# Performance work log

Hardware: AMD Instinct MI355X
Metric: run time of the kernel (lower is better)

## Reference

```python
import jax, jax.numpy as jnp
import numpy as np

LN_EPS = 1e-12


def setup_inputs() -> dict:
    key = jax.random.key(0)
    ks = jax.random.split(key, 5)
    E, H, I = 8, 768, 3072
    T = 2048  # tokens per expert (capacity-balanced)
    N = E * T
    return {
        "hidden_states": jax.random.normal(ks[0], (N, H), jnp.float32),
        "w1": jax.random.normal(ks[1], (E, H, I), jnp.float32) * (H ** -0.5),
        "b1": jax.random.normal(ks[2], (E, I), jnp.float32) * 0.02,
        "w2": jax.random.normal(ks[3], (E, I, H), jnp.float32) * (I ** -0.5),
        "b2": jax.random.normal(ks[4], (E, H), jnp.float32) * 0.02,
        "ln_gamma": jnp.ones((H,), jnp.float32),
        "ln_beta": jnp.zeros((H,), jnp.float32),
        "tokens_per_expert": T,
    }


def reference(hidden_states, w1, b1, w2, b2, ln_gamma, ln_beta, tokens_per_expert):
    E = w1.shape[0]
    N, H = hidden_states.shape
    # tokens are pre-sorted by expert; equal capacity per expert -> grouped GEMM
    x = hidden_states.reshape(E, tokens_per_expert, H)  # [E, T, H]
    # dense1 + exact GELU (BERT ACT2FN['gelu'])
    inter = jax.nn.gelu(jnp.einsum("eth,ehi->eti", x, w1) + b1[:, None, :],
                        approximate=False)  # [E, T, I]
    # dense2
    out = jnp.einsum("eti,eih->eth", inter, w2) + b2[:, None, :]  # [E, T, H]
    # dropout is identity in eval mode; residual + LayerNorm
    y = out.reshape(N, H) + hidden_states
    mean = jnp.mean(y, axis=-1, keepdims=True)
    var = jnp.mean(jnp.square(y - mean), axis=-1, keepdims=True)
    return (y - mean) * jax.lax.rsqrt(var + LN_EPS) * ln_gamma + ln_beta
```

## Files before the change

kernel.cpp:

```cpp
#include <hip/hip_runtime.h>
#include <hip/hip_bf16.h>
#include <math.h>

#define E_   8
#define H_   768
#define I_   3072
#define T_   2048
#define NTOK (E_ * T_)

typedef __attribute__((ext_vector_type(8))) short bf16x8;
typedef __attribute__((ext_vector_type(4))) float f32x4;

typedef __attribute__((address_space(3))) void lds_void;
typedef const __attribute__((address_space(1))) void gl_void;

__device__ __forceinline__ void gload16(const void* g, void* l) {
  __builtin_amdgcn_global_load_lds((gl_void*)g, (lds_void*)l, 16, 0, 0);
}

#define FENCE() asm volatile("" ::: "memory")
#define BAR()                         \
  do {                                \
    FENCE();                          \
    __builtin_amdgcn_s_barrier();     \
    FENCE();                          \
  } while (0)
#define VMWAIT(n) asm volatile("s_waitcnt vmcnt(" #n ")" ::: "memory")

#define MFMA16(a, b, c) __builtin_amdgcn_mfma_f32_16x16x32_bf16(a, b, c, 0, 0, 0)

__device__ __forceinline__ float gelu_fast(float v) {
  float inner = v * fmaf(v * v, 0.044715f, 1.0f);
  float e = __builtin_amdgcn_exp2f(inner * -2.3022082f);
  return v * __builtin_amdgcn_rcpf(1.0f + e);
}

__global__ __launch_bounds__(256) void cvt_bf16_kernel(
    const float* __restrict__ in, __hip_bfloat16* __restrict__ out) {
  int i = (blockIdx.x * 256 + threadIdx.x) * 4;
  float4 v = *(const float4*)(in + i);
  __align__(8) __hip_bfloat16 t[4];
  t[0] = __float2bfloat16(v.x);
  t[1] = __float2bfloat16(v.y);
  t[2] = __float2bfloat16(v.z);
  t[3] = __float2bfloat16(v.w);
  *(ushort4*)(out + i) = *(const ushort4*)t;
}

__global__ __launch_bounds__(256) void transpose_cvt_kernel(
    const float* __restrict__ src, __hip_bfloat16* __restrict__ dst,
    int R, int C) {
  __shared__ __hip_bfloat16 tile[64][65];
  int e  = blockIdx.z;
  int c0 = blockIdx.x * 64;
  int r0 = blockIdx.y * 64;
  const float* s = src + (size_t)e * R * C;
  __hip_bfloat16* d = dst + (size_t)e * R * C;
  int tx = threadIdx.x & 63, ty = threadIdx.x >> 6;
#pragma unroll
  for (int r = ty; r < 64; r += 4)
    tile[r][tx] = __float2bfloat16(s[(size_t)(r0 + r) * C + c0 + tx]);
  __syncthreads();
#pragma unroll
  for (int r = ty; r < 64; r += 4)
    d[(size_t)(c0 + r) * R + r0 + tx] = tile[tx][r];
}

template <int K, int N, bool GELU>
__global__ __launch_bounds__(512, 2) void gemm8p_kernel(
    const __hip_bfloat16* __restrict__ A,
    const __hip_bfloat16* __restrict__ B,
    const float* __restrict__ bias,
    __hip_bfloat16* __restrict__ out) {
  constexpr int MT = T_ / 256;
  constexpr int NT = N / 256;
  constexpr int KT = K / 64;

  __shared__ __hip_bfloat16 sA[2][2][128][64];
  __shared__ __hip_bfloat16 sB[2][2][128][64];

  int nwg = gridDim.x;
  int b0  = blockIdx.x;
  int bid = (b0 & 7) * (nwg >> 3) + (b0 >> 3);

  int e   = bid / (MT * NT);
  int rr_ = bid % (MT * NT);
  int bm  = rr_ / NT;
  int bn  = rr_ % NT;

  const __hip_bfloat16* Ae = A + (size_t)e * T_ * K + (size_t)bm * 256 * K;
  const __hip_bfloat16* Be = B + (size_t)e * N  * K + (size_t)bn * 256 * K;

  int tid  = threadIdx.x;
  int lane = tid & 63;
  int wid  = tid >> 6;
  int wr   = wid >> 2;
  int wc   = wid & 3;
  int l15  = lane & 15;
  int l16h = lane >> 4;

  int i0 = tid, i1 = 512 + tid;
  int lr0 = i0 >> 3, c80 = i0 & 7, cg0 = c80 ^ (lr0 & 7);
  int lr1 = i1 >> 3, c81 = i1 & 7, cg1 = c81 ^ (lr1 & 7);
  int rA0 = ((lr0 >> 6) << 7) | (lr0 & 63);
  int rA1 = ((lr1 >> 6) << 7) | (lr1 & 63);
  int rB0 = ((lr0 >> 5) << 6) | (lr0 & 31);
  int rB1 = ((lr1 >> 5) << 6) | (lr1 & 31);

  auto stageA = [&](int buf, int h, int kt) {
    const __hip_bfloat16* g = Ae + (size_t)kt * 64;
    gload16(g + (size_t)(rA0 | (h << 6)) * K + cg0 * 8, &sA[buf][h][lr0][c80 * 8]);
    gload16(g + (size_t)(rA1 | (h << 6)) * K + cg1 * 8, &sA[buf][h][lr1][c81 * 8]);
  };
  auto stageB = [&](int buf, int h, int kt) {
    const __hip_bfloat16* g = Be + (size_t)kt * 64;
    gload16(g + (size_t)(rB0 | (h << 5)) * K + cg0 * 8, &sB[buf][h][lr0][c80 * 8]);
    gload16(g + (size_t)(rB1 | (h << 5)) * K + cg1 * 8, &sB[buf][h][lr1][c81 * 8]);
  };

  int laBase = wr * 64 + l15;
  int lbBase = wc * 32 + l15;
  int s7   = l15 & 7;
  int cgr0 = ((0 | l16h) ^ s7) * 8;
  int cgr1 = ((4 | l16h) ^ s7) * 8;

  f32x4 acc[8][4] = {};
  bf16x8 af[4][2], bfv[4][2];

  stageA(0, 0, 0);
  stageB(0, 0, 0);
  stageB(0, 1, 0);
  stageA(0, 1, 0);

  auto ktile = [&](int kt, int p, bool pf) {
    VMWAIT(4);
    BAR();
#pragma unroll
    for (int mf = 0; mf < 4; ++mf) {
      int la = laBase + mf * 16;
      af[mf][0] = *(const bf16x8*)&sA[p][0][la][cgr0];
      af[mf][1] = *(const bf16x8*)&sA[p][0][la][cgr1];
    }
#pragma unroll
    for (int nf = 0; nf < 2; ++nf) {
      int lb = lbBase + nf * 16;
      bfv[nf][0] = *(const bf16x8*)&sB[p][0][lb][cgr0];
      bfv[nf][1] = *(const bf16x8*)&sB[p][0][lb][cgr1];
    }
    if (pf) stageA(p ^ 1, 0, kt + 1);
    __builtin_amdgcn_s_setprio(1);
#pragma unroll
    for (int mf = 0; mf < 4; ++mf)
#pragma unroll
      for (int nf = 0; nf < 2; ++nf) {
        acc[mf][nf] = MFMA16(af[mf][0], bfv[nf][0], acc[mf][nf]);
        acc[mf][nf] = MFMA16(af[mf][1], bfv[nf][1], acc[mf][nf]);
      }
    __builtin_amdgcn_s_setprio(0);
    if (pf) { VMWAIT(4); } else { VMWAIT(2); }
    BAR();
#pragma unroll
    for (int nf = 0; nf < 2; ++nf) {
      int lb = lbBase + nf * 16;
      bfv[2 + nf][0] = *(const bf16x8*)&sB[p][1][lb][cgr0];
      bfv[2 + nf][1] = *(const bf16x8*)&sB[p][1][lb][cgr1];
    }
    if (pf) stageB(p ^ 1, 0, kt + 1);
    __builtin_amdgcn_s_setprio(1);
#pragma unroll
    for (int mf = 0; mf < 4; ++mf)
#pragma unroll
      for (int nf = 2; nf < 4; ++nf) {
        acc[mf][nf] = MFMA16(af[mf][0], bfv[nf][0], acc[mf][nf]);
        acc[mf][nf] = MFMA16(af[mf][1], bfv[nf][1], acc[mf][nf]);
      }
    __builtin_amdgcn_s_setprio(0);
    if (pf) { VMWAIT(4); } else { VMWAIT(0); }
    BAR();
#pragma unroll
    for (int mf = 0; mf < 4; ++mf) {
      int la = laBase + mf * 16;
      af[mf][0] = *(const bf16x8*)&sA[p][1][la][cgr0];
      af[mf][1] = *(const bf16x8*)&sA[p][1][la][cgr1];
    }
    if (pf) stageB(p ^ 1, 1, kt + 1);
    __builtin_amdgcn_s_setprio(1);
#pragma unroll
    for (int mf = 0; mf < 4; ++mf)
#pragma unroll
      for (int nf = 2; nf < 4; ++nf) {
        acc[4 + mf][nf] = MFMA16(af[mf][0], bfv[nf][0], acc[4 + mf][nf]);
        acc[4 + mf][nf] = MFMA16(af[mf][1], bfv[nf][1], acc[4 + mf][nf]);
      }
    __builtin_amdgcn_s_setprio(0);
    if (pf) stageA(p ^ 1, 1, kt + 1);
    __builtin_amdgcn_s_setprio(1);
#pragma unroll
    for (int mf = 0; mf < 4; ++mf)
#pragma unroll
      for (int nf = 0; nf < 2; ++nf) {
        acc[4 + mf][nf] = MFMA16(af[mf][0], bfv[nf][0], acc[4 + mf][nf]);
        acc[4 + mf][nf] = MFMA16(af[mf][1], bfv[nf][1], acc[4 + mf][nf]);
      }
    __builtin_amdgcn_s_setprio(0);
  };

  int p = 0;
  for (int kt = 0; kt < KT - 1; ++kt) {
    ktile(kt, p, true);
    p ^= 1;
  }
  ktile(KT - 1, p, false);

  const float* be = bias + (size_t)e * N + bn * 256;
  __hip_bfloat16* oe =
      out + (size_t)e * T_ * N + (size_t)(bm * 256) * N + bn * 256;
  int r4 = l16h * 4;
#pragma unroll
  for (int mi = 0; mi < 8; ++mi) {
    int mh = mi >> 2, mf = mi & 3;
    int rowb = wr * 128 + mh * 64 + mf * 16 + r4;
#pragma unroll
    for (int nf = 0; nf < 4; ++nf) {
      int cc   = wc * 64 + nf * 16 + l15;
      float bv = be[cc];
#pragma unroll
      for (int r = 0; r < 4; ++r) {
        float v = acc[mi][nf][r] + bv;
        if (GELU) v = gelu_fast(v);
        oe[(size_t)(rowb + r) * N + cc] = __float2bfloat16(v);
      }
    }
  }
}

__global__ __launch_bounds__(256) void ln_kernel(
    const __hip_bfloat16* __restrict__ yraw, const float* __restrict__ x,
    const float* __restrict__ gamma, const float* __restrict__ beta,
    float* __restrict__ out) {
  int row  = blockIdx.x;
  int tid  = threadIdx.x;
  int lane = tid & 63, wid = tid >> 6;
  const __hip_bfloat16* yr = yraw + (size_t)row * H_;
  const float* xr = x + (size_t)row * H_;

  float v[3];
  float s = 0.f, s2 = 0.f;
#pragma unroll
  for (int j = 0; j < 3; ++j) {
    int c   = tid + j * 256;
    float t = __bfloat162float(yr[c]) + xr[c];
    v[j] = t;
    s += t;
    s2 += t * t;
  }
#pragma unroll
  for (int o = 32; o > 0; o >>= 1) {
    s  += __shfl_down(s, o);
    s2 += __shfl_down(s2, o);
  }
  __shared__ float ls[4], ls2[4];
  if (lane == 0) { ls[wid] = s; ls2[wid] = s2; }
  __syncthreads();
  float tot  = ls[0] + ls[1] + ls[2] + ls[3];
  float tot2 = ls2[0] + ls2[1] + ls2[2] + ls2[3];
  float mean = tot * (1.0f / 768.0f);
  float var  = tot2 * (1.0f / 768.0f) - mean * mean;
  float inv  = rsqrtf(var + 1e-12f);
  float* orow = out + (size_t)row * H_;
#pragma unroll
  for (int j = 0; j < 3; ++j) {
    int c = tid + j * 256;
    orow[c] = (v[j] - mean) * inv * gamma[c] + beta[c];
  }
}

extern "C" void kernel_launch(void* const* d_in, const int* in_sizes, int n_in,
                              void* d_out, int out_size, void* d_ws,
                              size_t ws_size, hipStream_t stream) {
  const float* x     = (const float*)d_in[0];
  const float* w1    = (const float*)d_in[1];
  const float* b1    = (const float*)d_in[2];
  const float* w2    = (const float*)d_in[3];
  const float* b2    = (const float*)d_in[4];
  const float* gamma = (const float*)d_in[5];
  const float* beta  = (const float*)d_in[6];
  float* out = (float*)d_out;

  char* ws = (char*)d_ws;
  __hip_bfloat16* w1t   = (__hip_bfloat16*)(ws);
  __hip_bfloat16* w2t   = (__hip_bfloat16*)(ws + 37748736);
  __hip_bfloat16* x_bf  = (__hip_bfloat16*)(ws + 75497472);
  __hip_bfloat16* inter = (__hip_bfloat16*)(ws + 100663296);
  __hip_bfloat16* yraw  = x_bf;

  cvt_bf16_kernel<<<(NTOK * H_) / (256 * 4), 256, 0, stream>>>(x, x_bf);
  transpose_cvt_kernel<<<dim3(I_ / 64, H_ / 64, E_), 256, 0, stream>>>(
      w1, w1t, H_, I_);
  transpose_cvt_kernel<<<dim3(H_ / 64, I_ / 64, E_), 256, 0, stream>>>(
      w2, w2t, I_, H_);
  gemm8p_kernel<H_, I_, true>
      <<<E_ * (T_ / 256) * (I_ / 256), 512, 0, stream>>>(x_bf, w1t, b1, inter);
  gemm8p_kernel<I_, H_, false>
      <<<E_ * (T_ / 256) * (H_ / 256), 512, 0, stream>>>(inter, w2t, b2, yraw);
  ln_kernel<<<NTOK, 256, 0, stream>>>(yraw, x, gamma, beta, out);
}
```

Measured before the change: 253.0 us.

## Restructure GEMM k-tile into two phases and use 256x192 tiles for dense2

The GEMM k-tile loop is reorganised from four phases with three barriers into two phases with two barriers. The whole B tile is staged at once and each wave's B fragments stay in registers across both A halves. The N tile width becomes a template parameter, and the second GEMM uses 192-wide tiles so its grid grows from 192 to 256 workgroups, better filling the CUs. The costs are more live B-fragment registers, different wait counts for prefetch overlap, and a smaller N tile for dense2, which lowers reuse.

Result: no change. 252.8 us (-0.1%).

```diff
diff --git a/kernel.cpp b/kernel.cpp
--- a/kernel.cpp
+++ b/kernel.cpp
@@ -66,18 +66,21 @@
     d[(size_t)(c0 + r) * R + r0 + tx] = tile[tx][r];
 }
 
-template <int K, int N, bool GELU>
-__global__ __launch_bounds__(512, 2) void gemm8p_kernel(
+template <int K, int N, int BN, bool GELU>
+__global__ __launch_bounds__(512, 2) void gemm2p_kernel(
     const __hip_bfloat16* __restrict__ A,
     const __hip_bfloat16* __restrict__ B,
     const float* __restrict__ bias,
     __hip_bfloat16* __restrict__ out) {
   constexpr int MT = T_ / 256;
-  constexpr int NT = N / 256;
+  constexpr int NT = N / BN;
   constexpr int KT = K / 64;
+  constexpr int NF = BN / 64;
+  constexpr int WCW = BN / 4;
+  constexpr int BPASS = BN / 64;
 
   __shared__ __hip_bfloat16 sA[2][2][128][64];
-  __shared__ __hip_bfloat16 sB[2][2][128][64];
+  __shared__ __hip_bfloat16 sB[2][BN][64];
 
   int nwg = gridDim.x;
   int b0  = blockIdx.x;
@@ -89,7 +92,7 @@
   int bn  = rr_ % NT;
 
   const __hip_bfloat16* Ae = A + (size_t)e * T_ * K + (size_t)bm * 256 * K;
-  const __hip_bfloat16* Be = B + (size_t)e * N  * K + (size_t)bn * 256 * K;
+  const __hip_bfloat16* Be = B + (size_t)e * N  * K + (size_t)bn * BN * K;
 
   int tid  = threadIdx.x;
   int lane = tid & 63;
@@ -104,36 +107,38 @@
   int lr1 = i1 >> 3, c81 = i1 & 7, cg1 = c81 ^ (lr1 & 7);
   int rA0 = ((lr0 >> 6) << 7) | (lr0 & 63);
   int rA1 = ((lr1 >> 6) << 7) | (lr1 & 63);
-  int rB0 = ((lr0 >> 5) << 6) | (lr0 & 31);
-  int rB1 = ((lr1 >> 5) << 6) | (lr1 & 31);
 
   auto stageA = [&](int buf, int h, int kt) {
     const __hip_bfloat16* g = Ae + (size_t)kt * 64;
     gload16(g + (size_t)(rA0 | (h << 6)) * K + cg0 * 8, &sA[buf][h][lr0][c80 * 8]);
     gload16(g + (size_t)(rA1 | (h << 6)) * K + cg1 * 8, &sA[buf][h][lr1][c81 * 8]);
   };
-  auto stageB = [&](int buf, int h, int kt) {
+  auto stageB = [&](int buf, int kt) {
     const __hip_bfloat16* g = Be + (size_t)kt * 64;
-    gload16(g + (size_t)(rB0 | (h << 5)) * K + cg0 * 8, &sB[buf][h][lr0][c80 * 8]);
-    gload16(g + (size_t)(rB1 | (h << 5)) * K + cg1 * 8, &sB[buf][h][lr1][c81 * 8]);
+#pragma unroll
+    for (int q = 0; q < BPASS; ++q) {
+      int idx = q * 512 + tid;
+      int lr = idx >> 3, c8 = idx & 7;
+      int cg = c8 ^ (lr & 7);
+      gload16(g + (size_t)lr * K + cg * 8, &sB[buf][lr][c8 * 8]);
+    }
   };
 
   int laBase = wr * 64 + l15;
-  int lbBase = wc * 32 + l15;
+  int lbBase = wc * WCW + l15;
   int s7   = l15 & 7;
   int cgr0 = ((0 | l16h) ^ s7) * 8;
   int cgr1 = ((4 | l16h) ^ s7) * 8;
 
-  f32x4 acc[8][4] = {};
-  bf16x8 af[4][2], bfv[4][2];
+  f32x4 acc[8][NF] = {};
+  bf16x8 af[4][2], bfv[NF][2];
 
   stageA(0, 0, 0);
-  stageB(0, 0, 0);
-  stageB(0, 1, 0);
+  stageB(0, 0);
   stageA(0, 1, 0);
 
   auto ktile = [&](int kt, int p, bool pf) {
-    VMWAIT(4);
+    VMWAIT(2);
     BAR();
 #pragma unroll
     for (int mf = 0; mf < 4; ++mf) {
@@ -142,40 +147,29 @@
       af[mf][1] = *(const bf16x8*)&sA[p][0][la][cgr1];
     }
 #pragma unroll
-    for (int nf = 0; nf < 2; ++nf) {
+    for (int nf = 0; nf < NF; ++nf) {
       int lb = lbBase + nf * 16;
-      bfv[nf][0] = *(const bf16x8*)&sB[p][0][lb][cgr0];
-      bfv[nf][1] = *(const bf16x8*)&sB[p][0][lb][cgr1];
-    }
-    if (pf) stageA(p ^ 1, 0, kt + 1);
+      bfv[nf][0] = *(const bf16x8*)&sB[p][lb][cgr0];
+      bfv[nf][1] = *(const bf16x8*)&sB[p][lb][cgr1];
+    }
+    if (pf) {
+      stageA(p ^ 1, 0, kt + 1);
+      stageB(p ^ 1, kt + 1);
+    }
     __builtin_amdgcn_s_setprio(1);
 #pragma unroll
     for (int mf = 0; mf < 4; ++mf)
 #pragma unroll
-      for (int nf = 0; nf < 2; ++nf) {
+      for (int nf = 0; nf < NF; ++nf) {
         acc[mf][nf] = MFMA16(af[mf][0], bfv[nf][0], acc[mf][nf]);
         acc[mf][nf] = MFMA16(af[mf][1], bfv[nf][1], acc[mf][nf]);
       }
     __builtin_amdgcn_s_setprio(0);
-    if (pf) { VMWAIT(4); } else { VMWAIT(2); }
-    BAR();
-#pragma unroll
-    for (int nf = 0; nf < 2; ++nf) {
-      int lb = lbBase + nf * 16;
-      bfv[2 + nf][0] = *(const bf16x8*)&sB[p][1][lb][cgr0];
-      bfv[2 + nf][1] = *(const bf16x8*)&sB[p][1][lb][cgr1];
-    }
-    if (pf) stageB(p ^ 1, 0, kt + 1);
-    __builtin_amdgcn_s_setprio(1);
-#pragma unroll
-    for (int mf = 0; mf < 4; ++mf)
-#pragma unroll
-      for (int nf = 2; nf < 4; ++nf) {
-        acc[mf][nf] = MFMA16(af[mf][0], bfv[nf][0], acc[mf][nf]);
-        acc[mf][nf] = MFMA16(af[mf][1], bfv[nf][1], acc[mf][nf]);
-      }
-    __builtin_amdgcn_s_setprio(0);
-    if (pf) { VMWAIT(4); } else { VMWAIT(0); }
+    if (pf) {
+      if constexpr (BN == 256) { VMWAIT(6); } else { VMWAIT(5); }
+    } else {
+      VMWAIT(0);
+    }
     BAR();
 #pragma unroll
     for (int mf = 0; mf < 4; ++mf) {
@@ -183,22 +177,12 @@
       af[mf][0] = *(const bf16x8*)&sA[p][1][la][cgr0];
       af[mf][1] = *(const bf16x8*)&sA[p][1][la][cgr1];
     }
-    if (pf) stageB(p ^ 1, 1, kt + 1);
-    __builtin_amdgcn_s_setprio(1);
-#pragma unroll
-    for (int mf = 0; mf < 4; ++mf)
-#pragma unroll
-      for (int nf = 2; nf < 4; ++nf) {
-        acc[4 + mf][nf] = MFMA16(af[mf][0], bfv[nf][0], acc[4 + mf][nf]);
-        acc[4 + mf][nf] = MFMA16(af[mf][1], bfv[nf][1], acc[4 + mf][nf]);
-      }
-    __builtin_amdgcn_s_setprio(0);
     if (pf) stageA(p ^ 1, 1, kt + 1);
     __builtin_amdgcn_s_setprio(1);
 #pragma unroll
     for (int mf = 0; mf < 4; ++mf)
 #pragma unroll
-      for (int nf = 0; nf < 2; ++nf) {
+      for (int nf = 0; nf < NF; ++nf) {
         acc[4 + mf][nf] = MFMA16(af[mf][0], bfv[nf][0], acc[4 + mf][nf]);
         acc[4 + mf][nf] = MFMA16(af[mf][1], bfv[nf][1], acc[4 + mf][nf]);
       }
@@ -212,17 +196,17 @@
   }
   ktile(KT - 1, p, false);
 
-  const float* be = bias + (size_t)e * N + bn * 256;
+  const float* be = bias + (size_t)e * N + bn * BN;
   __hip_bfloat16* oe =
-      out + (size_t)e * T_ * N + (size_t)(bm * 256) * N + bn * 256;
+      out + (size_t)e * T_ * N + (size_t)(bm * 256) * N + bn * BN;
   int r4 = l16h * 4;
 #pragma unroll
   for (int mi = 0; mi < 8; ++mi) {
     int mh = mi >> 2, mf = mi & 3;
     int rowb = wr * 128 + mh * 64 + mf * 16 + r4;
 #pragma unroll
-    for (int nf = 0; nf < 4; ++nf) {
-      int cc   = wc * 64 + nf * 16 + l15;
+    for (int nf = 0; nf < NF; ++nf) {
+      int cc   = wc * WCW + nf * 16 + l15;
       float bv = be[cc];
 #pragma unroll
       for (int r = 0; r < 4; ++r) {
@@ -299,9 +283,9 @@
       w1, w1t, H_, I_);
   transpose_cvt_kernel<<<dim3(H_ / 64, I_ / 64, E_), 256, 0, stream>>>(
       w2, w2t, I_, H_);
-  gemm8p_kernel<H_, I_, true>
+  gemm2p_kernel<H_, I_, 256, true>
       <<<E_ * (T_ / 256) * (I_ / 256), 512, 0, stream>>>(x_bf, w1t, b1, inter);
-  gemm8p_kernel<I_, H_, false>
-      <<<E_ * (T_ / 256) * (H_ / 256), 512, 0, stream>>>(inter, w2t, b2, yraw);
+  gemm2p_kernel<I_, H_, 192, false>
+      <<<E_ * (T_ / 256) * (H_ / 192), 512, 0, stream>>>(inter, w2t, b2, yraw);
   ln_kernel<<<NTOK, 256, 0, stream>>>(yraw, x, gamma, beta, out);
 }
```

## Restructure GEMM main loop into two-tile unrolled ping-pong schedule with explicit waits

Applied to the files above, without the earlier changes.

Replaces the single-k-tile loop with a two-k-tile unrolled iteration. Prefetch is issued for both buffers, and each quadrant of MFMAs is bracketed by barriers and explicit lgkmcnt waits with sched_barrier, in the style of an 8-wave ping-pong schedule. The goal is tighter overlap of global-to-LDS loads, LDS reads and MFMA, and more even instruction interleaving across the waves of the workgroup. Separately, the transpose kernel's write phase now stores two bf16 values per thread as ushort2, giving wider coalesced stores. The extra barriers could add sync overhead, and the kernel now requires an even k-tile count.

Result: slower. 258.3 us (+2.1%).

```diff
diff --git a/kernel.cpp b/kernel.cpp
--- a/kernel.cpp
+++ b/kernel.cpp
@@ -26,6 +26,11 @@
     FENCE();                          \
   } while (0)
 #define VMWAIT(n) asm volatile("s_waitcnt vmcnt(" #n ")" ::: "memory")
+#define LGKM0()                                  \
+  do {                                           \
+    asm volatile("s_waitcnt lgkmcnt(0)" ::: "memory"); \
+    __builtin_amdgcn_sched_barrier(0);           \
+  } while (0)
 
 #define MFMA16(a, b, c) __builtin_amdgcn_mfma_f32_16x16x32_bf16(a, b, c, 0, 0, 0)
 
@@ -61,20 +66,28 @@
   for (int r = ty; r < 64; r += 4)
     tile[r][tx] = __float2bfloat16(s[(size_t)(r0 + r) * C + c0 + tx]);
   __syncthreads();
-#pragma unroll
-  for (int r = ty; r < 64; r += 4)
-    d[(size_t)(c0 + r) * R + r0 + tx] = tile[tx][r];
+  int tx2 = threadIdx.x & 31;
+  int ty2 = threadIdx.x >> 5;
+#pragma unroll
+  for (int rr = ty2; rr < 64; rr += 8) {
+    ushort2 v;
+    v.x = *(const ushort*)&tile[2 * tx2][rr];
+    v.y = *(const ushort*)&tile[2 * tx2 + 1][rr];
+    *(ushort2*)&d[(size_t)(c0 + rr) * R + r0 + 2 * tx2] = v;
+  }
 }
 
 template <int K, int N, bool GELU>
-__global__ __launch_bounds__(512, 2) void gemm8p_kernel(
+__global__ __launch_bounds__(512, 2) void gemm8q_kernel(
     const __hip_bfloat16* __restrict__ A,
     const __hip_bfloat16* __restrict__ B,
     const float* __restrict__ bias,
     __hip_bfloat16* __restrict__ out) {
-  constexpr int MT = T_ / 256;
-  constexpr int NT = N / 256;
-  constexpr int KT = K / 64;
+  constexpr int MT  = T_ / 256;
+  constexpr int NT  = N / 256;
+  constexpr int KT  = K / 64;
+  constexpr int NIT = KT / 2;
+  static_assert(KT % 2 == 0, "even K-tile count required");
 
   __shared__ __hip_bfloat16 sA[2][2][128][64];
   __shared__ __hip_bfloat16 sB[2][2][128][64];
@@ -127,90 +140,82 @@
   f32x4 acc[8][4] = {};
   bf16x8 af[4][2], bfv[4][2];
 
+  auto readA = [&](int buf, int h) {
+#pragma unroll
+    for (int mf = 0; mf < 4; ++mf) {
+      int la = laBase + mf * 16;
+      af[mf][0] = *(const bf16x8*)&sA[buf][h][la][cgr0];
+      af[mf][1] = *(const bf16x8*)&sA[buf][h][la][cgr1];
+    }
+  };
+  auto readB = [&](int buf, int h) {
+#pragma unroll
+    for (int nf = 0; nf < 2; ++nf) {
+      int lb = lbBase + nf * 16;
+      bfv[2 * h + nf][0] = *(const bf16x8*)&sB[buf][h][lb][cgr0];
+      bfv[2 * h + nf][1] = *(const bf16x8*)&sB[buf][h][lb][cgr1];
+    }
+  };
+  auto mmaQ = [&](int mh, int nh) {
+    __builtin_amdgcn_s_setprio(1);
+#pragma unroll
+    for (int mf = 0; mf < 4; ++mf)
+#pragma unroll
+      for (int nf = 2 * nh; nf < 2 * nh + 2; ++nf) {
+        acc[4 * mh + mf][nf] = MFMA16(af[mf][0], bfv[nf][0], acc[4 * mh + mf][nf]);
+        acc[4 * mh + mf][nf] = MFMA16(af[mf][1], bfv[nf][1], acc[4 * mh + mf][nf]);
+      }
+    __builtin_amdgcn_s_setprio(0);
+  };
+
   stageA(0, 0, 0);
   stageB(0, 0, 0);
   stageB(0, 1, 0);
   stageA(0, 1, 0);
-
-  auto ktile = [&](int kt, int p, bool pf) {
-    VMWAIT(4);
-    BAR();
-#pragma unroll
-    for (int mf = 0; mf < 4; ++mf) {
-      int la = laBase + mf * 16;
-      af[mf][0] = *(const bf16x8*)&sA[p][0][la][cgr0];
-      af[mf][1] = *(const bf16x8*)&sA[p][0][la][cgr1];
-    }
-#pragma unroll
-    for (int nf = 0; nf < 2; ++nf) {
-      int lb = lbBase + nf * 16;
-      bfv[nf][0] = *(const bf16x8*)&sB[p][0][lb][cgr0];
-      bfv[nf][1] = *(const bf16x8*)&sB[p][0][lb][cgr1];
-    }
-    if (pf) stageA(p ^ 1, 0, kt + 1);
-    __builtin_amdgcn_s_setprio(1);
-#pragma unroll
-    for (int mf = 0; mf < 4; ++mf)
-#pragma unroll
-      for (int nf = 0; nf < 2; ++nf) {
-        acc[mf][nf] = MFMA16(af[mf][0], bfv[nf][0], acc[mf][nf]);
-        acc[mf][nf] = MFMA16(af[mf][1], bfv[nf][1], acc[mf][nf]);
-      }
-    __builtin_amdgcn_s_setprio(0);
-    if (pf) { VMWAIT(4); } else { VMWAIT(2); }
-    BAR();
-#pragma unroll
-    for (int nf = 0; nf < 2; ++nf) {
-      int lb = lbBase + nf * 16;
-      bfv[2 + nf][0] = *(const bf16x8*)&sB[p][1][lb][cgr0];
-      bfv[2 + nf][1] = *(const bf16x8*)&sB[p][1][lb][cgr1];
-    }
-    if (pf) stageB(p ^ 1, 0, kt + 1);
-    __builtin_amdgcn_s_setprio(1);
-#pragma unroll
-    for (int mf = 0; mf < 4; ++mf)
-#pragma unroll
-      for (int nf = 2; nf < 4; ++nf) {
-        acc[mf][nf] = MFMA16(af[mf][0], bfv[nf][0], acc[mf][nf]);
-        acc[mf][nf] = MFMA16(af[mf][1], bfv[nf][1], acc[mf][nf]);
-      }
-    __builtin_amdgcn_s_setprio(0);
-    if (pf) { VMWAIT(4); } else { VMWAIT(0); }
-    BAR();
-#pragma unroll
-    for (int mf = 0; mf < 4; ++mf) {
-      int la = laBase + mf * 16;
-      af[mf][0] = *(const bf16x8*)&sA[p][1][la][cgr0];
-      af[mf][1] = *(const bf16x8*)&sA[p][1][la][cgr1];
-    }
-    if (pf) stageB(p ^ 1, 1, kt + 1);
-    __builtin_amdgcn_s_setprio(1);
-#pragma unroll
-    for (int mf = 0; mf < 4; ++mf)
-#pragma unroll
-      for (int nf = 2; nf < 4; ++nf) {
-        acc[4 + mf][nf] = MFMA16(af[mf][0], bfv[nf][0], acc[4 + mf][nf]);
-        acc[4 + mf][nf] = MFMA16(af[mf][1], bfv[nf][1], acc[4 + mf][nf]);
-      }
-    __builtin_amdgcn_s_setprio(0);
-    if (pf) stageA(p ^ 1, 1, kt + 1);
-    __builtin_amdgcn_s_setprio(1);
-#pragma unroll
-    for (int mf = 0; mf < 4; ++mf)
-#pragma unroll
-      for (int nf = 0; nf < 2; ++nf) {
-        acc[4 + mf][nf] = MFMA16(af[mf][0], bfv[nf][0], acc[4 + mf][nf]);
-        acc[4 + mf][nf] = MFMA16(af[mf][1], bfv[nf][1], acc[4 + mf][nf]);
-      }
-    __builtin_amdgcn_s_setprio(0);
-  };
-
-  int p = 0;
-  for (int kt = 0; kt < KT - 1; ++kt) {
-    ktile(kt, p, true);
-    p ^= 1;
-  }
-  ktile(KT - 1, p, false);
+  stageA(1, 0, 1);
+  stageB(1, 0, 1);
+  stageB(1, 1, 1);
+  VMWAIT(6);
+  BAR();
+
+  auto iter = [&](int t0, bool pf) {
+    readA(0, 0);
+    readB(0, 0);
+    stageA(1, 1, t0 + 1);
+    BAR(); LGKM0(); mmaQ(0, 0); BAR();
+    readB(0, 1);
+    if (pf) stageA(0, 0, t0 + 2);
+    BAR(); LGKM0(); mmaQ(0, 1); BAR();
+    readA(0, 1);
+    if (pf) stageB(0, 0, t0 + 2);
+    BAR(); LGKM0(); mmaQ(1, 1); BAR();
+    if (pf) {
+      stageB(0, 1, t0 + 2);
+      VMWAIT(6);
+    } else {
+      VMWAIT(2);
+    }
+    BAR(); mmaQ(1, 0); BAR();
+    readA(1, 0);
+    readB(1, 0);
+    if (pf) stageA(0, 1, t0 + 2);
+    BAR(); LGKM0(); mmaQ(0, 0); BAR();
+    readB(1, 1);
+    if (pf) stageA(1, 0, t0 + 3);
+    else VMWAIT(0);
+    BAR(); LGKM0(); mmaQ(0, 1); BAR();
+    readA(1, 1);
+    if (pf) stageB(1, 0, t0 + 3);
+    BAR(); LGKM0(); mmaQ(1, 1); BAR();
+    if (pf) {
+      stageB(1, 1, t0 + 3);
+      VMWAIT(6);
+    }
+    BAR(); mmaQ(1, 0); BAR();
+  };
+
+  for (int it = 0; it < NIT - 1; ++it) iter(2 * it, true);
+  iter(2 * (NIT - 1), false);
 
   const float* be = bias + (size_t)e * N + bn * 256;
   __hip_bfloat16* oe =
@@ -299,9 +304,9 @@
       w1, w1t, H_, I_);
   transpose_cvt_kernel<<<dim3(H_ / 64, I_ / 64, E_), 256, 0, stream>>>(
       w2, w2t, I_, H_);
-  gemm8p_kernel<H_, I_, true>
+  gemm8q_kernel<H_, I_, true>
       <<<E_ * (T_ / 256) * (I_ / 256), 512, 0, stream>>>(x_bf, w1t, b1, inter);
-  gemm8p_kernel<I_, H_, false>
+  gemm8q_kernel<I_, H_, false>
       <<<E_ * (T_ / 256) * (H_ / 256), 512, 0, stream>>>(inter, w2t, b2, yraw);
   ln_kernel<<<NTOK, 256, 0, stream>>>(yraw, x, gamma, beta, out);
 }
```
